# Optimization experiments

Hardware: AMD Instinct MI355X
Metric: run time of the kernel (lower is better)

## Reference

```python
import jax, jax.numpy as jnp
import numpy as np

N = 100000      # nodes
E = 600000      # edges
IN, OUT = 128, 32
L1 = IN - (IN - OUT) // 3          # 96
L2 = IN - (2 * (IN - OUT)) // 3    # 64


def setup_inputs() -> dict:
    key = jax.random.key(0)
    ks = jax.random.split(key, 12)

    def lin(k, i, o):
        return jax.random.normal(k, (i, o), jnp.float32) / np.float32(np.sqrt(i))

    return {
        "x": jax.random.normal(ks[0], (N, IN), jnp.float32),
        "edge_index": jax.random.randint(ks[1], (2, E), 0, N, dtype=jnp.int32),
        # ClusterGCNConv 1: lin_out (W,b) + lin_root (no bias)
        "W1": lin(ks[2], IN, L1), "b1": jnp.zeros((L1,), jnp.float32), "Wr1": lin(ks[3], IN, L1),
        # ClusterGCNConv 2
        "W2": lin(ks[4], L1, L2), "b2": jnp.zeros((L2,), jnp.float32), "Wr2": lin(ks[5], L1, L2),
        # GCNConv mu / logstd heads
        "Wmu": lin(ks[6], L2, OUT), "bmu": jnp.zeros((OUT,), jnp.float32),
        "Wls": lin(ks[7], L2, OUT), "bls": jnp.zeros((OUT,), jnp.float32),
    }


def _with_self_loops(edge_index, n):
    loops = jnp.arange(n, dtype=edge_index.dtype)
    src = jnp.concatenate([edge_index[0], loops])
    dst = jnp.concatenate([edge_index[1], loops])
    return src, dst


def _cluster_gcn(x, edge_index, W, b, Wr, n):
    # PyG ClusterGCNConv (diag_lambda=0): out = (D^{-1} (A+I)) x @ W + b + x @ Wr
    src, dst = _with_self_loops(edge_index, n)
    deg = jax.ops.segment_sum(jnp.ones_like(dst, x.dtype), dst, num_segments=n)
    dinv = 1.0 / jnp.clip(deg, 1.0)
    agg = jax.ops.segment_sum(x[src] * dinv[dst][:, None], dst, num_segments=n)
    return agg @ W + b + x @ Wr


def _gcn(x, edge_index, W, b, n):
    # PyG GCNConv: h = x @ W; out = D^{-1/2} (A+I) D^{-1/2} h + b
    h = x @ W
    src, dst = _with_self_loops(edge_index, n)
    deg = jax.ops.segment_sum(jnp.ones_like(dst, h.dtype), dst, num_segments=n)
    dis = jax.lax.rsqrt(jnp.clip(deg, 1.0))  # deg >= 1 thanks to self loops
    norm = dis[src] * dis[dst]
    return jax.ops.segment_sum(h[src] * norm[:, None], dst, num_segments=n) + b


def reference(x, edge_index, W1, b1, Wr1, W2, b2, Wr2, Wmu, bmu, Wls, bls):
    n = x.shape[0]
    h = jax.nn.relu(_cluster_gcn(x, edge_index, W1, b1, Wr1, n))
    h = jax.nn.relu(_cluster_gcn(h, edge_index, W2, b2, Wr2, n))
    return (_gcn(h, edge_index, Wmu, bmu, n), _gcn(h, edge_index, Wls, bls, n))
```

## Files before the change

### kernel.cpp

```cpp
#include <hip/hip_runtime.h>

#define TPB 256
#define GTPB 512

typedef __attribute__((ext_vector_type(8))) short          bf8_t;
typedef __attribute__((ext_vector_type(8))) unsigned short us8_t;
typedef __attribute__((ext_vector_type(4))) float          f4_t;
typedef __attribute__((ext_vector_type(4))) unsigned short us4_t;

__device__ __forceinline__ unsigned short f2bf(float f) {
    union { float f; unsigned u; } v; v.f = f;
    unsigned r = v.u + 0x7FFFu + ((v.u >> 16) & 1u);
    return (unsigned short)(r >> 16);
}
__device__ __forceinline__ float bf2f(unsigned short u) {
    union { unsigned u; float f; } v; v.u = (unsigned)u << 16; return v.f;
}


__global__ void k_count(const int* __restrict__ ei, int E, int* __restrict__ cnt) {
    int e = blockIdx.x * TPB + threadIdx.x;
    if (e < E) atomicAdd(&cnt[ei[E + e]], 1);
}

__global__ void k_blocksum(const int* __restrict__ cnt, int n, int* __restrict__ bsum) {
    __shared__ int s[TPB];
    int t = threadIdx.x, i = blockIdx.x * TPB + t;
    s[t] = (i < n) ? cnt[i] : 0;
    __syncthreads();
    for (int off = TPB / 2; off > 0; off >>= 1) {
        if (t < off) s[t] += s[t + off];
        __syncthreads();
    }
    if (t == 0) bsum[blockIdx.x] = s[0];
}

__global__ void k_scan_bsum(int* __restrict__ bsum, int nb) {
    __shared__ int s[512];
    int t = threadIdx.x;
    int v = (t < nb) ? bsum[t] : 0;
    s[t] = v; __syncthreads();
    for (int off = 1; off < 512; off <<= 1) {
        int x = (t >= off) ? s[t - off] : 0;
        __syncthreads();
        s[t] += x;
        __syncthreads();
    }
    if (t < nb) bsum[t] = s[t] - v;
}

__global__ void k_rowptr(const int* __restrict__ cnt, const int* __restrict__ bsum, int n, int E,
                         int* __restrict__ rowptr, int* __restrict__ cursor,
                         float* __restrict__ dinv, float* __restrict__ dis) {
    __shared__ int s[TPB];
    int t = threadIdx.x, i = blockIdx.x * TPB + t;
    int v = (i < n) ? cnt[i] : 0;
    s[t] = v; __syncthreads();
    for (int off = 1; off < TPB; off <<= 1) {
        int x = (t >= off) ? s[t - off] : 0;
        __syncthreads();
        s[t] += x;
        __syncthreads();
    }
    if (i < n) {
        int start = bsum[blockIdx.x] + s[t] - v;
        rowptr[i] = start;
        cursor[i] = start;
        float d = (float)(v + 1);
        dinv[i] = 1.0f / d;
        dis[i]  = rsqrtf(d);
    }
    if (i == 0) rowptr[n] = E;
}

__global__ void k_fill(const int* __restrict__ ei, int E,
                       int* __restrict__ cursor, int* __restrict__ col) {
    int e = blockIdx.x * TPB + threadIdx.x;
    if (e < E) {
        int src = ei[e], dst = ei[E + e];
        int p = atomicAdd(&cursor[dst], 1);
        col[p] = src;
    }
}

__global__ void k_wconv(const float* W1, const float* Wr1, const float* W2, const float* Wr2,
                        const float* Wmu, const float* Wls,
                        unsigned short* T1, unsigned short* Tr1, unsigned short* T2,
                        unsigned short* Tr2, unsigned short* Tmu, unsigned short* Tls) {
    const float* W; unsigned short* T; int K, M;
    switch (blockIdx.y) {
        case 0: W = W1;  T = T1;  K = 128; M = 96; break;
        case 1: W = Wr1; T = Tr1; K = 128; M = 96; break;
        case 2: W = W2;  T = T2;  K = 96;  M = 64; break;
        case 3: W = Wr2; T = Tr2; K = 96;  M = 64; break;
        case 4: W = Wmu; T = Tmu; K = 64;  M = 32; break;
        default:W = Wls; T = Tls; K = 64;  M = 32; break;
    }
    int idx = blockIdx.x * TPB + threadIdx.x;
    if (idx < K * M) {
        int m = idx / K, k = idx % K;
        T[idx] = f2bf(W[k * M + m]);
    }
}

template <int K, int M, bool AF32>
__global__ __launch_bounds__(GTPB) void k_gemm4(const void* __restrict__ Av,
                                                const unsigned short* __restrict__ WT,
                                                unsigned short* __restrict__ Yb,
                                                int n, int nt) {
    constexpr int KS = K / 32;
    constexpr int ST = K + 8;
    __shared__ unsigned short Bs[M * ST];
    for (int i = threadIdx.x * 8; i < M * K; i += GTPB * 8) {
        int m = i / K, k = i - m * K;
        *(us8_t*)(Bs + m * ST + k) = *(const us8_t*)(WT + i);
    }
    __syncthreads();

    int lane = threadIdx.x & 63;
    int wave = threadIdx.x >> 6;
    int quad = lane >> 4;
    int l15  = lane & 15;

    for (int tile = blockIdx.x; tile < nt; tile += gridDim.x) {
        int base = tile * 128 + wave * 16;
        int rA = base + l15; if (rA > n - 1) rA = n - 1;

        bf8_t a[KS];
        if (AF32) {
            const float* ap = (const float*)Av + (size_t)rA * K + quad * 8;
#pragma unroll
            for (int s = 0; s < KS; s++) {
                f4_t lo = *(const f4_t*)(ap + s * 32);
                f4_t hi = *(const f4_t*)(ap + s * 32 + 4);
                bf8_t t;
                t[0] = (short)f2bf(lo.x); t[1] = (short)f2bf(lo.y);
                t[2] = (short)f2bf(lo.z); t[3] = (short)f2bf(lo.w);
                t[4] = (short)f2bf(hi.x); t[5] = (short)f2bf(hi.y);
                t[6] = (short)f2bf(hi.z); t[7] = (short)f2bf(hi.w);
                a[s] = t;
            }
        } else {
            const unsigned short* ap = (const unsigned short*)Av + (size_t)rA * K + quad * 8;
#pragma unroll
            for (int s = 0; s < KS; s++) a[s] = *(const bf8_t*)(ap + s * 32);
        }

        int row = base + quad * 4;
#pragma unroll
        for (int ct = 0; ct < M / 16; ct++) {
            const unsigned short* bp = Bs + (ct * 16 + l15) * ST + quad * 8;
            f4_t acc = {0.f, 0.f, 0.f, 0.f};
#pragma unroll
            for (int s = 0; s < KS; s++) {
                bf8_t b = *(const bf8_t*)(bp + s * 32);
                acc = __builtin_amdgcn_mfma_f32_16x16x32_bf16(a[s], b, acc, 0, 0, 0);
            }
            int colg = ct * 16 + l15;
#pragma unroll
            for (int r = 0; r < 4; r++) {
                if (row + r < n) Yb[(size_t)(row + r) * M + colg] = f2bf(acc[r]);
            }
        }
    }
}

__global__ __launch_bounds__(GTPB) void k_gemm_out4(const unsigned short* __restrict__ Z,
                                                    const unsigned short* __restrict__ WT,
                                                    const float* __restrict__ bmu,
                                                    const float* __restrict__ bls,
                                                    float* __restrict__ out, int n, int nt) {
    constexpr int K = 64, M = 64, KS = 2, ST = K + 8;
    __shared__ unsigned short Bs[M * ST];
    for (int i = threadIdx.x * 8; i < M * K; i += GTPB * 8) {
        int m = i / K, k = i - m * K;
        *(us8_t*)(Bs + m * ST + k) = *(const us8_t*)(WT + i);
    }
    __syncthreads();

    int lane = threadIdx.x & 63;
    int wave = threadIdx.x >> 6;
    int quad = lane >> 4;
    int l15  = lane & 15;

    for (int tile = blockIdx.x; tile < nt; tile += gridDim.x) {
        int base = tile * 128 + wave * 16;
        int rA = base + l15; if (rA > n - 1) rA = n - 1;
        const unsigned short* ap = Z + (size_t)rA * K + quad * 8;
        bf8_t a[KS];
#pragma unroll
        for (int s = 0; s < KS; s++) a[s] = *(const bf8_t*)(ap + s * 32);

        int row = base + quad * 4;
#pragma unroll
        for (int ct = 0; ct < M / 16; ct++) {
            const unsigned short* bp = Bs + (ct * 16 + l15) * ST + quad * 8;
            f4_t acc = {0.f, 0.f, 0.f, 0.f};
#pragma unroll
            for (int s = 0; s < KS; s++) {
                bf8_t b = *(const bf8_t*)(bp + s * 32);
                acc = __builtin_amdgcn_mfma_f32_16x16x32_bf16(a[s], b, acc, 0, 0, 0);
            }
            int colg = ct * 16 + l15;
            float bias = (colg < 32) ? bmu[colg] : bls[colg - 32];
            float* dst = (colg < 32) ? (out + colg) : (out + (size_t)n * 32 + (colg - 32));
#pragma unroll
            for (int r = 0; r < 4; r++) {
                if (row + r < n) dst[(size_t)(row + r) * 32] = acc[r] + bias;
            }
        }
    }
}

template <int MF, int GRP, bool SCALE>
__global__ __launch_bounds__(TPB) void k_aggc(const unsigned short* __restrict__ AB,
                                              const float* __restrict__ bias,
                                              const float* __restrict__ dinv,
                                              const float* __restrict__ dis,
                                              const int* __restrict__ rowptr,
                                              const int* __restrict__ col,
                                              unsigned short* __restrict__ Hb, int n) {
    constexpr int LD = 2 * MF;
    int g = blockIdx.x * (TPB / GRP) + threadIdx.x / GRP;
    int l = threadIdx.x & (GRP - 1);
    if (g >= n) return;
    int c = l * 8;
    if (c >= MF) return;
    int r0 = rowptr[g], r1 = rowptr[g + 1];
    float acc[8];
    {
        bf8_t v = *(const bf8_t*)(AB + (size_t)g * LD + c);
#pragma unroll
        for (int j = 0; j < 8; j++) acc[j] = bf2f((unsigned short)v[j]);
    }
    int e = r0;
    for (; e + 4 <= r1; e += 4) {
        int s0 = col[e], s1 = col[e + 1], s2 = col[e + 2], s3 = col[e + 3];
        bf8_t v0 = *(const bf8_t*)(AB + (size_t)s0 * LD + c);
        bf8_t v1 = *(const bf8_t*)(AB + (size_t)s1 * LD + c);
        bf8_t v2 = *(const bf8_t*)(AB + (size_t)s2 * LD + c);
        bf8_t v3 = *(const bf8_t*)(AB + (size_t)s3 * LD + c);
#pragma unroll
        for (int j = 0; j < 8; j++)
            acc[j] += (bf2f((unsigned short)v0[j]) + bf2f((unsigned short)v1[j]))
                    + (bf2f((unsigned short)v2[j]) + bf2f((unsigned short)v3[j]));
    }
    for (; e < r1; ++e) {
        int s = col[e];
        bf8_t v = *(const bf8_t*)(AB + (size_t)s * LD + c);
#pragma unroll
        for (int j = 0; j < 8; j++) acc[j] += bf2f((unsigned short)v[j]);
    }
    float di = dinv[g];
    float sc = SCALE ? dis[g] : 1.0f;
    bf8_t rr = *(const bf8_t*)(AB + (size_t)g * LD + MF + c);
    us8_t o;
#pragma unroll
    for (int j = 0; j < 8; j++) {
        float h = fmaxf(acc[j] * di + bf2f((unsigned short)rr[j]) + bias[c + j], 0.f);
        o[j] = f2bf(SCALE ? sc * h : h);
    }
    *(us8_t*)(Hb + (size_t)g * MF + c) = o;
}

__global__ __launch_bounds__(TPB) void k_agghead(const unsigned short* __restrict__ H2s,
                                                 const float* __restrict__ dis,
                                                 const int* __restrict__ rowptr,
                                                 const int* __restrict__ col,
                                                 unsigned short* __restrict__ Z, int n) {
    const int GRP = 8;
    int g = blockIdx.x * (TPB / GRP) + threadIdx.x / GRP;
    int l = threadIdx.x & (GRP - 1);
    if (g >= n) return;
    int c = l * 8;
    int r0 = rowptr[g], r1 = rowptr[g + 1];
    float acc[8];
    {
        bf8_t v = *(const bf8_t*)(H2s + (size_t)g * 64 + c);
#pragma unroll
        for (int j = 0; j < 8; j++) acc[j] = bf2f((unsigned short)v[j]);
    }
    int e = r0;
    for (; e + 4 <= r1; e += 4) {
        int s0 = col[e], s1 = col[e + 1], s2 = col[e + 2], s3 = col[e + 3];
        bf8_t v0 = *(const bf8_t*)(H2s + (size_t)s0 * 64 + c);
        bf8_t v1 = *(const bf8_t*)(H2s + (size_t)s1 * 64 + c);
        bf8_t v2 = *(const bf8_t*)(H2s + (size_t)s2 * 64 + c);
        bf8_t v3 = *(const bf8_t*)(H2s + (size_t)s3 * 64 + c);
#pragma unroll
        for (int j = 0; j < 8; j++)
            acc[j] += (bf2f((unsigned short)v0[j]) + bf2f((unsigned short)v1[j]))
                    + (bf2f((unsigned short)v2[j]) + bf2f((unsigned short)v3[j]));
    }
    for (; e < r1; ++e) {
        int s = col[e];
        bf8_t v = *(const bf8_t*)(H2s + (size_t)s * 64 + c);
#pragma unroll
        for (int j = 0; j < 8; j++) acc[j] += bf2f((unsigned short)v[j]);
    }
    float dg = dis[g];
    us8_t o;
#pragma unroll
    for (int j = 0; j < 8; j++) o[j] = f2bf(dg * acc[j]);
    *(us8_t*)(Z + (size_t)g * 64 + c) = o;
}


extern "C" void kernel_launch(void* const* d_in, const int* in_sizes, int n_in,
                              void* d_out, int out_size, void* d_ws, size_t ws_size,
                              hipStream_t stream) {
    const float* x   = (const float*)d_in[0];
    const int*   ei  = (const int*)d_in[1];
    const float* W1  = (const float*)d_in[2];
    const float* b1  = (const float*)d_in[3];
    const float* Wr1 = (const float*)d_in[4];
    const float* W2  = (const float*)d_in[5];
    const float* b2  = (const float*)d_in[6];
    const float* Wr2 = (const float*)d_in[7];
    const float* Wmu = (const float*)d_in[8];
    const float* bmu = (const float*)d_in[9];
    const float* Wls = (const float*)d_in[10];
    const float* bls = (const float*)d_in[11];
    float* out = (float*)d_out;

    const int IN = 128, L1F = 96, L2F = 64;
    const int N = in_sizes[0] / IN;
    const int E = in_sizes[1] / 2;

    char* ws = (char*)d_ws;
    size_t off = 0;
    auto alloc = [&](size_t b) { size_t r = off; off += (b + 255) & ~(size_t)255; return r; };

    const int nb = (N + TPB - 1) / TPB;
    int*   cnt  = (int*)(ws + alloc((size_t)N * 4));
    int*   bsum = (int*)(ws + alloc((size_t)nb * 4));
    int*   rowp = (int*)(ws + alloc((size_t)(N + 1) * 4));
    int*   curs = (int*)(ws + alloc((size_t)N * 4));
    int*   col  = (int*)(ws + alloc((size_t)E * 4));
    float* dinv = (float*)(ws + alloc((size_t)N * 4));
    float* dis  = (float*)(ws + alloc((size_t)N * 4));
    unsigned short* T1  = (unsigned short*)(ws + alloc((size_t)IN  * L1F * 2));
    unsigned short* Tr1 = (unsigned short*)(ws + alloc((size_t)IN  * L1F * 2));
    unsigned short* T2  = (unsigned short*)(ws + alloc((size_t)L1F * L2F * 2));
    unsigned short* Tr2 = (unsigned short*)(ws + alloc((size_t)L1F * L2F * 2));
    unsigned short* Tmu = (unsigned short*)(ws + alloc((size_t)L2F * 32 * 2));
    unsigned short* Tls = (unsigned short*)(ws + alloc((size_t)L2F * 32 * 2));
    unsigned short* AB1 = (unsigned short*)(ws + alloc((size_t)N * 2 * L1F * 2));
    unsigned short* AB2 = (unsigned short*)(ws + alloc((size_t)N * 2 * L2F * 2));
    unsigned short* Hb1 = (unsigned short*)(ws + alloc((size_t)N * L1F * 2));
    unsigned short* H2s = (unsigned short*)(ws + alloc((size_t)N * L2F * 2));
    unsigned short* Zag = (unsigned short*)(ws + alloc((size_t)N * L2F * 2));

    hipMemsetAsync(cnt, 0, (size_t)N * 4, stream);

    dim3 eg((E + TPB - 1) / TPB);
    k_count<<<eg, TPB, 0, stream>>>(ei, E, cnt);
    k_blocksum<<<nb, TPB, 0, stream>>>(cnt, N, bsum);
    k_scan_bsum<<<1, 512, 0, stream>>>(bsum, nb);
    k_rowptr<<<nb, TPB, 0, stream>>>(cnt, bsum, N, E, rowp, curs, dinv, dis);
    k_fill<<<eg, TPB, 0, stream>>>(ei, E, curs, col);

    k_wconv<<<dim3(48, 6), TPB, 0, stream>>>(W1, Wr1, W2, Wr2, Wmu, Wls,
                                             T1, Tr1, T2, Tr2, Tmu, Tls);

    const int nt = (N + 127) / 128;
    k_gemm4<128, 192, true><<<768, GTPB, 0, stream>>>(x, T1, AB1, N, nt);
    k_aggc<96, 16, false><<<(N + 15) / 16, TPB, 0, stream>>>(AB1, b1, dinv, dis, rowp, col, Hb1, N);

    k_gemm4<96, 128, false><<<768, GTPB, 0, stream>>>(Hb1, T2, AB2, N, nt);
    k_aggc<64, 8, true><<<(N + 31) / 32, TPB, 0, stream>>>(AB2, b2, dinv, dis, rowp, col, H2s, N);

    k_agghead<<<(N + 31) / 32, TPB, 0, stream>>>(H2s, dis, rowp, col, Zag, N);
    k_gemm_out4<<<768, GTPB, 0, stream>>>(Zag, Tmu, bmu, bls, out, N, nt);
}
```

Baseline: 292.0 us.

## Split GEMM outputs into separate Y/R buffers and pack aggregation threads densely

The GEMM kernels now write the neighbour-transform half and the root half into two separate row-compact buffers instead of one interleaved buffer. This lets the gather in aggregation touch denser rows with better cache-line use. Layer-1 aggregation uses 12 lanes per node with a flat index mapping, so no threads sit idle on the column guard. Launch bounds, unroll factors and grid sizes (one block per tile) are also adjusted. The risks are more register pressure from the bound of 6 blocks and the cost of the integer divide by 12.

```diff
diff --git a/kernel.cpp b/kernel.cpp
--- a/kernel.cpp
+++ b/kernel.cpp
@@ -104,12 +104,14 @@
 }
 
 template <int K, int M, bool AF32>
-__global__ __launch_bounds__(GTPB) void k_gemm4(const void* __restrict__ Av,
-                                                const unsigned short* __restrict__ WT,
-                                                unsigned short* __restrict__ Yb,
-                                                int n, int nt) {
+__global__ __launch_bounds__(GTPB, 6) void k_gemm5(const void* __restrict__ Av,
+                                                   const unsigned short* __restrict__ WT,
+                                                   unsigned short* __restrict__ Y,
+                                                   unsigned short* __restrict__ R,
+                                                   int n, int nt) {
     constexpr int KS = K / 32;
     constexpr int ST = K + 8;
+    constexpr int MF = M / 2;
     __shared__ unsigned short Bs[M * ST];
     for (int i = threadIdx.x * 8; i < M * K; i += GTPB * 8) {
         int m = i / K, k = i - m * K;
@@ -147,7 +149,7 @@
         }
 
         int row = base + quad * 4;
-#pragma unroll
+#pragma unroll 3
         for (int ct = 0; ct < M / 16; ct++) {
             const unsigned short* bp = Bs + (ct * 16 + l15) * ST + quad * 8;
             f4_t acc = {0.f, 0.f, 0.f, 0.f};
@@ -157,19 +159,20 @@
                 acc = __builtin_amdgcn_mfma_f32_16x16x32_bf16(a[s], b, acc, 0, 0, 0);
             }
             int colg = ct * 16 + l15;
+            unsigned short* dst = (colg < MF) ? (Y + colg) : (R + (colg - MF));
 #pragma unroll
             for (int r = 0; r < 4; r++) {
-                if (row + r < n) Yb[(size_t)(row + r) * M + colg] = f2bf(acc[r]);
+                if (row + r < n) dst[(size_t)(row + r) * MF] = f2bf(acc[r]);
             }
         }
     }
 }
 
-__global__ __launch_bounds__(GTPB) void k_gemm_out4(const unsigned short* __restrict__ Z,
-                                                    const unsigned short* __restrict__ WT,
-                                                    const float* __restrict__ bmu,
-                                                    const float* __restrict__ bls,
-                                                    float* __restrict__ out, int n, int nt) {
+__global__ __launch_bounds__(GTPB, 6) void k_gemm_out5(const unsigned short* __restrict__ Z,
+                                                       const unsigned short* __restrict__ WT,
+                                                       const float* __restrict__ bmu,
+                                                       const float* __restrict__ bls,
+                                                       float* __restrict__ out, int n, int nt) {
     constexpr int K = 64, M = 64, KS = 2, ST = K + 8;
     __shared__ unsigned short Bs[M * ST];
     for (int i = threadIdx.x * 8; i < M * K; i += GTPB * 8) {
@@ -192,7 +195,7 @@
         for (int s = 0; s < KS; s++) a[s] = *(const bf8_t*)(ap + s * 32);
 
         int row = base + quad * 4;
-#pragma unroll
+#pragma unroll 2
         for (int ct = 0; ct < M / 16; ct++) {
             const unsigned short* bp = Bs + (ct * 16 + l15) * ST + quad * 8;
             f4_t acc = {0.f, 0.f, 0.f, 0.f};
@@ -213,33 +216,33 @@
 }
 
 template <int MF, int GRP, bool SCALE>
-__global__ __launch_bounds__(TPB) void k_aggc(const unsigned short* __restrict__ AB,
+__global__ __launch_bounds__(TPB) void k_aggc(const unsigned short* __restrict__ Y,
+                                              const unsigned short* __restrict__ R,
                                               const float* __restrict__ bias,
                                               const float* __restrict__ dinv,
                                               const float* __restrict__ dis,
                                               const int* __restrict__ rowptr,
                                               const int* __restrict__ col,
                                               unsigned short* __restrict__ Hb, int n) {
-    constexpr int LD = 2 * MF;
-    int g = blockIdx.x * (TPB / GRP) + threadIdx.x / GRP;
-    int l = threadIdx.x & (GRP - 1);
+    int idx = blockIdx.x * TPB + threadIdx.x;
+    int g = idx / GRP;
+    int l = idx - g * GRP;
     if (g >= n) return;
     int c = l * 8;
-    if (c >= MF) return;
     int r0 = rowptr[g], r1 = rowptr[g + 1];
     float acc[8];
     {
-        bf8_t v = *(const bf8_t*)(AB + (size_t)g * LD + c);
+        bf8_t v = *(const bf8_t*)(Y + (size_t)g * MF + c);
 #pragma unroll
         for (int j = 0; j < 8; j++) acc[j] = bf2f((unsigned short)v[j]);
     }
     int e = r0;
     for (; e + 4 <= r1; e += 4) {
         int s0 = col[e], s1 = col[e + 1], s2 = col[e + 2], s3 = col[e + 3];
-        bf8_t v0 = *(const bf8_t*)(AB + (size_t)s0 * LD + c);
-        bf8_t v1 = *(const bf8_t*)(AB + (size_t)s1 * LD + c);
-        bf8_t v2 = *(const bf8_t*)(AB + (size_t)s2 * LD + c);
-        bf8_t v3 = *(const bf8_t*)(AB + (size_t)s3 * LD + c);
+        bf8_t v0 = *(const bf8_t*)(Y + (size_t)s0 * MF + c);
+        bf8_t v1 = *(const bf8_t*)(Y + (size_t)s1 * MF + c);
+        bf8_t v2 = *(const bf8_t*)(Y + (size_t)s2 * MF + c);
+        bf8_t v3 = *(const bf8_t*)(Y + (size_t)s3 * MF + c);
 #pragma unroll
         for (int j = 0; j < 8; j++)
             acc[j] += (bf2f((unsigned short)v0[j]) + bf2f((unsigned short)v1[j]))
@@ -247,13 +250,13 @@
     }
     for (; e < r1; ++e) {
         int s = col[e];
-        bf8_t v = *(const bf8_t*)(AB + (size_t)s * LD + c);
+        bf8_t v = *(const bf8_t*)(Y + (size_t)s * MF + c);
 #pragma unroll
         for (int j = 0; j < 8; j++) acc[j] += bf2f((unsigned short)v[j]);
     }
     float di = dinv[g];
     float sc = SCALE ? dis[g] : 1.0f;
-    bf8_t rr = *(const bf8_t*)(AB + (size_t)g * LD + MF + c);
+    bf8_t rr = *(const bf8_t*)(R + (size_t)g * MF + c);
     us8_t o;
 #pragma unroll
     for (int j = 0; j < 8; j++) {
@@ -345,8 +348,10 @@
     unsigned short* Tr2 = (unsigned short*)(ws + alloc((size_t)L1F * L2F * 2));
     unsigned short* Tmu = (unsigned short*)(ws + alloc((size_t)L2F * 32 * 2));
     unsigned short* Tls = (unsigned short*)(ws + alloc((size_t)L2F * 32 * 2));
-    unsigned short* AB1 = (unsigned short*)(ws + alloc((size_t)N * 2 * L1F * 2));
-    unsigned short* AB2 = (unsigned short*)(ws + alloc((size_t)N * 2 * L2F * 2));
+    unsigned short* Y1  = (unsigned short*)(ws + alloc((size_t)N * L1F * 2));
+    unsigned short* R1  = (unsigned short*)(ws + alloc((size_t)N * L1F * 2));
+    unsigned short* Y2  = (unsigned short*)(ws + alloc((size_t)N * L2F * 2));
+    unsigned short* R2  = (unsigned short*)(ws + alloc((size_t)N * L2F * 2));
     unsigned short* Hb1 = (unsigned short*)(ws + alloc((size_t)N * L1F * 2));
     unsigned short* H2s = (unsigned short*)(ws + alloc((size_t)N * L2F * 2));
     unsigned short* Zag = (unsigned short*)(ws + alloc((size_t)N * L2F * 2));
@@ -364,12 +369,14 @@
                                              T1, Tr1, T2, Tr2, Tmu, Tls);
 
     const int nt = (N + 127) / 128;
-    k_gemm4<128, 192, true><<<768, GTPB, 0, stream>>>(x, T1, AB1, N, nt);
-    k_aggc<96, 16, false><<<(N + 15) / 16, TPB, 0, stream>>>(AB1, b1, dinv, dis, rowp, col, Hb1, N);
-
-    k_gemm4<96, 128, false><<<768, GTPB, 0, stream>>>(Hb1, T2, AB2, N, nt);
-    k_aggc<64, 8, true><<<(N + 31) / 32, TPB, 0, stream>>>(AB2, b2, dinv, dis, rowp, col, H2s, N);
+    k_gemm5<128, 192, true><<<nt, GTPB, 0, stream>>>(x, T1, Y1, R1, N, nt);
+    k_aggc<96, 12, false><<<((size_t)N * 12 + TPB - 1) / TPB, TPB, 0, stream>>>(
+        Y1, R1, b1, dinv, dis, rowp, col, Hb1, N);
+
+    k_gemm5<96, 128, false><<<nt, GTPB, 0, stream>>>(Hb1, T2, Y2, R2, N, nt);
+    k_aggc<64, 8, true><<<((size_t)N * 8 + TPB - 1) / TPB, TPB, 0, stream>>>(
+        Y2, R2, b2, dinv, dis, rowp, col, H2s, N);
 
     k_agghead<<<(N + 31) / 32, TPB, 0, stream>>>(H2s, dis, rowp, col, Zag, N);
-    k_gemm_out4<<<768, GTPB, 0, stream>>>(Zag, Tmu, bmu, bls, out, N, nt);
-}
+    k_gemm_out5<<<nt, GTPB, 0, stream>>>(Zag, Tmu, bmu, bls, out, N, nt);
+}
```

Measured after the change: 321.3 us. 1.1x slower.
